# Performance work log

Measured on AMD Instinct MI355X. Metric: run time of the kernel, lower is better.

## Reference

```python
import jax, jax.numpy as jnp
import numpy as np

NEG = -65504.0  # torch.finfo(float16).min
EPS = 1e-6

B, T, D = 2, 1024, 2048
H, HD = 16, 128          # n_head, head_dim
K = 128                  # dynamic_w_hidden_dim
IH = 1                   # dynamic_hidden_dim = H // squeeze_ratio


def _rope(x, freqs_cis):
    # x: [B,T,H,hd]; 'half' mode: first/second half are the rotation pair,
    # output is interleaved (stack(...,-1).flatten(3) in torch).
    half = x.shape[-1] // 2
    a, b = x[..., :half], x[..., half:]
    cos = freqs_cis[None, :, None, :, 0]
    sin = freqs_cis[None, :, None, :, 1]
    out = jnp.stack([a * cos - b * sin, b * cos + a * sin], axis=-1)
    return out.reshape(x.shape)


def _cross_head_proj(inputs, qw1, qw2, kw1, kw2, qdd, kdd):
    # inputs: [B,N,T,S]; qw1/qw2: [B,T,I,N]; kw1/kw2: [B,S,I,N]; qdd: [B,T,N]; kdd: [B,S,N]
    out = inputs
    out = out + jnp.einsum('bnts,btin,btim->bmts', inputs, qw1, qw2)
    out = out + jnp.einsum('bnts,bsin,bsim->bmts', inputs, kw1, kw2)
    out = out + inputs * jnp.swapaxes(qdd, 1, 2)[..., None]   # [B,N,T,1]
    out = out + inputs * jnp.swapaxes(kdd, 1, 2)[:, :, None, :]  # [B,N,1,S]
    return out


def setup_inputs() -> dict:
    key = jax.random.key(0)
    ks = jax.random.split(key, 7)
    x = jax.random.normal(ks[0], (B, T, D), jnp.float32)
    mask = jnp.tril(jnp.ones((1, 1, T, T), bool))  # causal
    # rotary tables: [T, hd/2, 2] (cos, sin)
    inv = 1.0 / (10000.0 ** (jnp.arange(0, HD, 2, dtype=jnp.float32) / HD))
    ang = jnp.arange(T, dtype=jnp.float32)[:, None] * inv[None, :]
    freqs_cis = jnp.stack([jnp.cos(ang), jnp.sin(ang)], axis=-1)
    s = 0.02
    wqkv = jax.random.normal(ks[1], (D, 3 * H * HD), jnp.float32) * s
    wo = jax.random.normal(ks[2], (H * HD, D), jnp.float32) * s
    dw1 = jax.random.normal(ks[3], (D, 4, K), jnp.float32) * s
    qkw = jax.random.normal(ks[4], (4, K, 2 * IH, H), jnp.float32) * s
    dd_w = jax.random.normal(ks[5], (D, 4 * H), jnp.float32) * s
    return {"x": x, "mask": mask, "freqs_cis": freqs_cis, "wqkv": wqkv,
            "wo": wo, "dw1": dw1, "qkw": qkw, "dd_w": dd_w}


def reference(x, mask, freqs_cis, wqkv, wo, dw1, qkw, dd_w):
    b, t, d = x.shape
    qkv = x @ wqkv
    q, k, v = jnp.split(qkv, [H * HD, 2 * H * HD], axis=-1)
    q = q.reshape(b, t, H, HD)
    k = k.reshape(b, t, H, HD)
    v = v.reshape(b, t, H, HD)
    q = _rope(q, freqs_cis)
    k = _rope(k, freqs_cis)
    q = jnp.swapaxes(q, 1, 2) * (HD ** -0.5)  # [B,H,T,hd]
    k = jnp.swapaxes(k, 1, 2)
    v = jnp.swapaxes(v, 1, 2)

    # ---- DynamicWeightProjection (G=1, squeezed) ----
    dw_hidden = jax.nn.gelu(jnp.einsum('btd,dck->btck', x, dw1), approximate=False)
    w = jnp.einsum('btck,ckim->btcim', dw_hidden, qkw)  # [B,T,4,2*IH,H]
    w1, w2 = w[..., :IH, :], w[..., IH:, :]
    w1 = w1 * jax.lax.rsqrt(jnp.mean(w1 * w1, axis=-1, keepdims=True) + EPS)
    pre_qw1, pre_kw1, post_qw1, post_kw1 = [w1[:, :, i] for i in range(4)]
    pre_qw2, pre_kw2, post_qw2, post_kw2 = [w2[:, :, i] for i in range(4)]
    dd = jnp.tanh(x @ dd_w).reshape(b, t, 4, H)
    pre_qdd, pre_kdd, post_qdd, post_kdd = [dd[:, :, i] for i in range(4)]

    # ---- attention with cross-head mixing ----
    logits = jnp.einsum('bhtd,bhsd->bhts', q, k)
    logits = _cross_head_proj(logits, pre_qw1, pre_qw2, pre_kw1, pre_kw2, pre_qdd, pre_kdd)
    logits = jnp.where(mask, logits, NEG)
    probs = jax.nn.softmax(logits, axis=-1)
    probs = _cross_head_proj(probs, post_qw1, post_qw2, post_kw1, post_kw2, post_qdd, post_kdd)
    o = jnp.einsum('bhts,bhsd->bhtd', probs, v)
    o = jnp.swapaxes(o, 1, 2).reshape(b, t, H * HD)
    return o @ wo
```

## Files before the change

kernel.cpp:

```cpp
#include <hip/hip_runtime.h>


typedef unsigned short u16;
typedef unsigned int u32;
typedef __attribute__((ext_vector_type(8))) short s16x8;
typedef __attribute__((ext_vector_type(4))) float f32x4;
typedef __attribute__((ext_vector_type(2))) float f32x2;
typedef __attribute__((ext_vector_type(2))) u16 u16x2;
typedef __attribute__((ext_vector_type(8))) u16 u16x8;

#define DEV __device__ __forceinline__

DEV float bf2f(u16 u) { union { u32 u; float f; } a; a.u = ((u32)u) << 16; return a.f; }
DEV u16 f2bf(float f) {
  union { float f; u32 u; } a; a.f = f;
  u32 r = a.u + 0x7fffu + ((a.u >> 16) & 1u);
  return (u16)(r >> 16);
}

DEV void gload16(const void* g, void* l) {
  __builtin_amdgcn_global_load_lds((__attribute__((address_space(1))) void*)g,
                                   (__attribute__((address_space(3))) void*)l,
                                   16, 0, 0);
}

template <int OUTBF>
__global__ __launch_bounds__(1024, 1) void gemm256(
    const u16* __restrict__ A, const u16* __restrict__ B, void* __restrict__ Cp,
    int K, int lda, int ldb, int ldc)
{
  __shared__ u16 sA[2][256 * 64];
  __shared__ u16 sB[2][256 * 64];
  const int tid = threadIdx.x, ln = tid & 63;
  const int wid = tid >> 6, wm = wid >> 2, wn = wid & 3;

  const int nx = gridDim.x;
  const int fid = blockIdx.y * nx + blockIdx.x;
  const int cpx = (nx * gridDim.y) >> 3;
  const int nid = (fid & 7) * cpx + (fid >> 3);
  const int bx = nid % nx, by = nid / nx;

  const u16* Ab = A + (size_t)(by * 256) * lda;
  const u16* Bb = B + (size_t)(bx * 256) * ldb;

  f32x4 acc[4][4];
#pragma unroll
  for (int m = 0; m < 4; ++m)
#pragma unroll
    for (int n = 0; n < 4; ++n) {
      f32x4 zz = {0.f, 0.f, 0.f, 0.f};
      acc[m][n] = zz;
    }

  int srow[2], scol[2], soff[2];
#pragma unroll
  for (int i = 0; i < 2; ++i) {
    int o = i * 16384 + tid * 16;
    soff[i] = o;
    int r = o >> 7;
    srow[i] = r;
    scol[i] = ((o & 127) ^ ((r & 7) << 4)) >> 1;
  }

#define STAGE_A(ba, k0)                                                   \
  {                                                                       \
    _Pragma("unroll")                                                     \
    for (int i_ = 0; i_ < 2; ++i_)                                        \
      gload16(Ab + (size_t)srow[i_] * lda + (k0) + scol[i_],              \
              (char*)(ba) + soff[i_]);                                    \
  }
#define STAGE_B(bb, k0)                                                   \
  {                                                                       \
    _Pragma("unroll")                                                     \
    for (int i_ = 0; i_ < 2; ++i_)                                        \
      gload16(Bb + (size_t)srow[i_] * ldb + (k0) + scol[i_],              \
              (char*)(bb) + soff[i_]);                                    \
  }

  const int arow = wm * 64 + (ln & 15);
  const int brow = wn * 64 + (ln & 15);
  const int kb = (ln >> 4) * 16;
  const int frswz = (ln & 7) << 4;
  const int NT = K >> 6;

  STAGE_A(sA[0], 0); STAGE_B(sB[0], 0);
  STAGE_A(sA[1], 64); STAGE_B(sB[1], 64);

  for (int t = 0; t < NT; ++t) {
    const int c = t & 1;
    asm volatile("s_waitcnt vmcnt(4)" ::: "memory");
    __builtin_amdgcn_s_barrier();
    const char* pa = (const char*)sA[c];
    const char* pb = (const char*)sB[c];
    s16x8 bfr[4][2];
#pragma unroll
    for (int n = 0; n < 4; ++n)
#pragma unroll
      for (int kk = 0; kk < 2; ++kk)
        bfr[n][kk] = *(const s16x8*)(pb + (size_t)(brow + n * 16) * 128 + ((kk * 64 + kb) ^ frswz));
#pragma unroll
    for (int ph = 0; ph < 4; ++ph) {
      s16x8 afr[2];
#pragma unroll
      for (int kk = 0; kk < 2; ++kk)
        afr[kk] = *(const s16x8*)(pa + (size_t)(arow + ph * 16) * 128 + ((kk * 64 + kb) ^ frswz));
      __builtin_amdgcn_s_setprio(1);
#pragma unroll
      for (int n = 0; n < 4; ++n)
#pragma unroll
        for (int kk = 0; kk < 2; ++kk)
          acc[ph][n] = __builtin_amdgcn_mfma_f32_16x16x32_bf16(
              afr[kk], bfr[n][kk], acc[ph][n], 0, 0, 0);
      __builtin_amdgcn_s_setprio(0);
    }
    __builtin_amdgcn_s_barrier();
    if (t + 2 < NT) { STAGE_A(sA[c], (t + 2) * 64); STAGE_B(sB[c], (t + 2) * 64); }
  }
#undef STAGE_A
#undef STAGE_B

  const int r0 = by * 256 + wm * 64 + ((ln >> 4) << 2);
  const int c0 = bx * 256 + wn * 64 + (ln & 15);
#pragma unroll
  for (int m = 0; m < 4; ++m)
#pragma unroll
    for (int n = 0; n < 4; ++n)
#pragma unroll
      for (int j = 0; j < 4; ++j) {
        int row = r0 + m * 16 + j, col = c0 + n * 16;
        if (OUTBF)
          ((u16*)Cp)[(size_t)row * ldc + col] = f2bf(acc[m][n][j]);
        else
          ((float*)Cp)[(size_t)row * ldc + col] = acc[m][n][j];
      }
}

template <int OUTBF>
__global__ __launch_bounds__(256) void gemm_bt(
    const u16* __restrict__ A, const u16* __restrict__ B, void* __restrict__ Cp,
    int K, int lda, int ldb, int ldc,
    long sAb, long sBb, long sCb1, long sCb2, int CZ2, int cmode, int swz)
{
  int bx = blockIdx.x, by = blockIdx.y;
  if (swz) {
    int nx = gridDim.x;
    int fid = by * nx + bx;
    int cpx = (nx * gridDim.y) >> 3;
    int nid = (fid & 7) * cpx + (fid >> 3);
    bx = nid % nx; by = nid / nx;
  }
  if (cmode == 1 && bx > by) return;
  __shared__ u16 sA[128 * 64];
  __shared__ u16 sB[128 * 64];
  const int tid = threadIdx.x, wv = tid >> 6, ln = tid & 63;
  const int z = blockIdx.z;
  const u16* Ab = A + (size_t)z * sAb + (size_t)(by * 128) * lda;
  const u16* Bb = B + (size_t)z * sBb + (size_t)(bx * 128) * ldb;
  const int wr = (wv >> 1) * 64, wc = (wv & 1) * 64;
  const int Keff = (cmode == 2) ? min(K, (by + 1) * 128) : K;

  f32x4 acc[4][4];
#pragma unroll
  for (int m = 0; m < 4; ++m)
#pragma unroll
    for (int n = 0; n < 4; ++n) {
      f32x4 zz = {0.f, 0.f, 0.f, 0.f};
      acc[m][n] = zz;
    }

  int o_[4], r_[4], cb_[4];
#pragma unroll
  for (int i = 0; i < 4; ++i) {
    int o = (wv * 4 + i) * 1024 + ln * 16;
    o_[i] = o;
    int r = o >> 7;
    r_[i] = r;
    cb_[i] = (o & 127) ^ ((r & 7) << 4);
  }
  const int frswz = (ln & 7) << 4;
  const int fkcol = (ln >> 4) << 4;

  for (int k0 = 0; k0 < Keff; k0 += 64) {
    __syncthreads();
#pragma unroll
    for (int i = 0; i < 4; ++i)
      gload16(Ab + (size_t)r_[i] * lda + (k0 + (cb_[i] >> 1)), (char*)sA + o_[i]);
#pragma unroll
    for (int i = 0; i < 4; ++i)
      gload16(Bb + (size_t)r_[i] * ldb + (k0 + (cb_[i] >> 1)), (char*)sB + o_[i]);
    __syncthreads();

#pragma unroll
    for (int ks = 0; ks < 2; ++ks) {
      s16x8 av[4], bv[4];
#pragma unroll
      for (int m = 0; m < 4; ++m) {
        int row = wr + m * 16 + (ln & 15);
        int addr = row * 128 + ((ks * 64 + fkcol) ^ frswz);
        av[m] = *(const s16x8*)((const char*)sA + addr);
      }
#pragma unroll
      for (int n = 0; n < 4; ++n) {
        int row = wc + n * 16 + (ln & 15);
        int addr = row * 128 + ((ks * 64 + fkcol) ^ frswz);
        bv[n] = *(const s16x8*)((const char*)sB + addr);
      }
#pragma unroll
      for (int m = 0; m < 4; ++m)
#pragma unroll
        for (int n = 0; n < 4; ++n)
          acc[m][n] = __builtin_amdgcn_mfma_f32_16x16x32_bf16(av[m], bv[n], acc[m][n], 0, 0, 0);
    }
  }

  const size_t cbase = (size_t)(z / CZ2) * sCb1 + (size_t)(z % CZ2) * sCb2;
  const int r0 = by * 128 + wr + ((ln >> 4) << 2);
  const int c0 = bx * 128 + wc + (ln & 15);
#pragma unroll
  for (int m = 0; m < 4; ++m)
#pragma unroll
    for (int n = 0; n < 4; ++n)
#pragma unroll
      for (int j = 0; j < 4; ++j) {
        int row = r0 + m * 16 + j, col = c0 + n * 16;
        if (OUTBF)
          ((u16*)Cp)[cbase + (size_t)row * ldc + col] = f2bf(acc[m][n][j]);
        else
          ((float*)Cp)[cbase + (size_t)row * ldc + col] = acc[m][n][j];
      }
}

template <int INBF>
__global__ __launch_bounds__(256) void transpose_to_bf16(
    const void* __restrict__ srcv, u16* __restrict__ dst,
    int R, int C, int Cpad, int srcLd, long sSrc1, long sSrc2, int Z2, long sDst)
{
  __shared__ float tile[32][33];
  const int z = blockIdx.z, z1 = z / Z2, z2 = z % Z2;
  const size_t sbase = (size_t)z1 * sSrc1 + (size_t)z2 * sSrc2;
  u16* d = dst + (size_t)z * sDst;
  const int c0 = blockIdx.x * 32, r0 = blockIdx.y * 32;
  const int tx = threadIdx.x, ty = threadIdx.y;
#pragma unroll
  for (int i = 0; i < 4; ++i) {
    int r = r0 + ty + i * 8, c = c0 + tx;
    float v = 0.f;
    if (c < C && r < R) {
      if (INBF) v = bf2f(((const u16*)srcv)[sbase + (size_t)r * srcLd + c]);
      else      v = ((const float*)srcv)[sbase + (size_t)r * srcLd + c];
    }
    tile[ty + i * 8][tx] = v;
  }
  __syncthreads();
#pragma unroll
  for (int i = 0; i < 4; ++i) {
    int dr = c0 + ty + i * 8, dc = r0 + tx;
    if (dr < Cpad && dc < R) d[(size_t)dr * R + dc] = f2bf(tile[tx][ty + i * 8]);
  }
}

__global__ void cvt_f32_bf16_k(const float* __restrict__ src, u16* __restrict__ dst, int n4) {
  int i = blockIdx.x * 256 + threadIdx.x;
  if (i >= n4) return;
  const float4 v = ((const float4*)src)[i];
  u16* o = dst + (size_t)i * 4;
  o[0] = f2bf(v.x); o[1] = f2bf(v.y); o[2] = f2bf(v.z); o[3] = f2bf(v.w);
}

__global__ __launch_bounds__(256) void rope_k(
    const u16* __restrict__ qkvm, const float* __restrict__ fc,
    u16* __restrict__ qb, u16* __restrict__ kb)
{
  const int bt = blockIdx.x, b = bt >> 10, t = bt & 1023;
  const u16* row = qkvm + (size_t)bt * 6912;
  const float SC = 0.08838834764831845f;
#pragma unroll
  for (int it = 0; it < 4; ++it) {
    int idx = threadIdx.x + it * 256;
    int h = idx >> 6, j = idx & 63;
    float c = fc[(t * 64 + j) * 2], sn = fc[(t * 64 + j) * 2 + 1];
    float qa = bf2f(row[h * 128 + j]), qbv = bf2f(row[h * 128 + 64 + j]);
    float ka = bf2f(row[2048 + h * 128 + j]), kbv = bf2f(row[2048 + h * 128 + 64 + j]);
    size_t o = ((size_t)(b * 16 + h) * 1024 + t) * 128 + 2 * j;
    qb[o]     = f2bf((qa * c - qbv * sn) * SC);
    qb[o + 1] = f2bf((qbv * c + qa * sn) * SC);
    kb[o]     = f2bf(ka * c - kbv * sn);
    kb[o + 1] = f2bf(kbv * c + ka * sn);
  }
}

__global__ __launch_bounds__(64) void gelu_bf16_k(u16* __restrict__ qm) {
  int bt = blockIdx.x, tid = threadIdx.x;
  u16* p = qm + (size_t)bt * 6912 + 6144 + tid * 8;
  u16x8 v = *(u16x8*)p;
#pragma unroll
  for (int i = 0; i < 8; ++i) {
    float f = bf2f(v[i]);
    f = 0.5f * f * (1.f + erff(f * 0.70710678118654752f));
    v[i] = f2bf(f);
  }
  *(u16x8*)p = v;
}

__global__ __launch_bounds__(64) void wproj_k(
    const u16* __restrict__ qkvm, const float* __restrict__ qkw,
    float* __restrict__ w1a, float* __restrict__ w2a, float* __restrict__ kpT)
{
  const int bt = blockIdx.x, ln = threadIdx.x;
  const int c = ln >> 4, m = ln & 15;
  const int b = bt >> 10, t = bt & 1023;
  const u16* hp = qkvm + (size_t)bt * 6912 + 6144 + c * 128;
  const float* Wp = qkw + (size_t)c * 4096 + m;
  float w1 = 0.f, w2 = 0.f;
  for (int k = 0; k < 128; ++k) {
    float hv = bf2f(hp[k]);
    w1 += hv * Wp[k * 32];
    w2 += hv * Wp[k * 32 + 16];
  }
  float ss = w1 * w1;
  ss += __shfl_xor(ss, 1); ss += __shfl_xor(ss, 2);
  ss += __shfl_xor(ss, 4); ss += __shfl_xor(ss, 8);
  float nrm = rsqrtf(ss * (1.f / 16.f) + 1e-6f);
  float w1n = w1 * nrm;
  size_t o = (size_t)bt * 64 + c * 16 + m;
  w1a[o] = w1n;
  w2a[o] = w2;
  size_t kb = (size_t)b * 98304 + (size_t)m * 1024 + t;
  if (c == 1) { kpT[kb] = w1n; kpT[kb + 16384] = w2; }
  if (c == 3) { kpT[kb + 49152] = w1n; kpT[kb + 65536] = w2; }
}

__global__ __launch_bounds__(64) void dd_k(const u16* __restrict__ qkvm,
                                           float* __restrict__ dda, float* __restrict__ kpT) {
  int bt = blockIdx.x, ln = threadIdx.x;
  int c = ln >> 4, m = ln & 15;
  int b = bt >> 10, t = bt & 1023;
  float v = tanhf(bf2f(qkvm[(size_t)bt * 6912 + 6656 + ln]));
  dda[(size_t)bt * 64 + ln] = v;
  size_t kb = (size_t)b * 98304 + (size_t)m * 1024 + t;
  if (c == 1) kpT[kb + 32768] = v;
  if (c == 3) kpT[kb + 81920] = v;
}

__global__ __launch_bounds__(512, 4) void proj_softmax_k(
    const u16* __restrict__ L, u16* __restrict__ P,
    const float* __restrict__ w1a, const float* __restrict__ w2a,
    const float* __restrict__ dda, const float* __restrict__ kparT)
{
  const int t = blockIdx.x, b = blockIdx.y;
  const int tid = threadIdx.x, wv = tid >> 6, ln = tid & 63;
  const int s0 = tid * 2;
  const bool live = (s0 <= t);
  const int sKeff = (t & ~127) + 128;

  __shared__ float tbuf[8][64][17];
  __shared__ float qpar[6][16];
  __shared__ float red2[16][8];
  __shared__ float rzf[16];
  if (tid < 96) {
    int a = tid >> 4, hh = tid & 15;
    const float* sp = (a == 0 || a == 3) ? w1a : ((a == 1 || a == 4) ? w2a : dda);
    int cc = (a < 3) ? 0 : 2;
    qpar[a][hh] = sp[(size_t)(b * 1024 + t) * 64 + cc * 16 + hh];
  }
  __syncthreads();

  const float* kp = kparT + (size_t)b * 98304 + s0;
  float v[16][2];
  const size_t lbase = ((size_t)(b * 16) * 1024 + t) * 1024 + s0;

  if (live) {
#pragma unroll
    for (int h = 0; h < 16; ++h) {
      u16x2 d = *(const u16x2*)(L + lbase + (size_t)h * 1048576);
      v[h][0] = bf2f(d[0]); v[h][1] = bf2f(d[1]);
    }
    float dq0 = 0.f, dq1 = 0.f, dk0 = 0.f, dk1 = 0.f;
#pragma unroll
    for (int h = 0; h < 16; ++h) {
      f32x2 k1 = *(const f32x2*)(kp + h * 1024);
      dq0 += v[h][0] * qpar[0][h]; dq1 += v[h][1] * qpar[0][h];
      dk0 += v[h][0] * k1[0];      dk1 += v[h][1] * k1[1];
    }
    const bool ok1 = (s0 + 1 <= t);
#pragma unroll
    for (int h = 0; h < 16; ++h) {
      f32x2 k2 = *(const f32x2*)(kp + 16384 + h * 1024);
      f32x2 kd = *(const f32x2*)(kp + 32768 + h * 1024);
      float a0 = v[h][0] * (1.f + qpar[2][h] + kd[0]) + qpar[1][h] * dq0 + k2[0] * dk0;
      float a1 = v[h][1] * (1.f + qpar[2][h] + kd[1]) + qpar[1][h] * dq1 + k2[1] * dk1;
      v[h][0] = __expf(a0);
      v[h][1] = ok1 ? __expf(a1) : 0.f;
    }
  }

  {
    float* tb = &tbuf[wv][ln][0];
#pragma unroll
    for (int h = 0; h < 16; ++h)
      tb[h] = live ? (v[h][0] + v[h][1]) : 0.f;
    int hh = ln & 15, q = ln >> 4;
    float sum = 0.f;
#pragma unroll
    for (int k = 0; k < 16; ++k) sum += tbuf[wv][q * 16 + k][hh];
    sum += __shfl_xor(sum, 16);
    sum += __shfl_xor(sum, 32);
    if (ln < 16) red2[ln][wv] = sum;
  }
  __syncthreads();
  if (tid < 16)
    rzf[tid] = 1.f / (((red2[tid][0] + red2[tid][1]) + (red2[tid][2] + red2[tid][3])) +
                      ((red2[tid][4] + red2[tid][5]) + (red2[tid][6] + red2[tid][7])));
  __syncthreads();

  if (s0 >= sKeff) return;

  const size_t pbase = ((size_t)(b * 16) * 1024 + t) * 1024 + s0;
  if (live) {
    float pdq0 = 0.f, pdq1 = 0.f, pdk0 = 0.f, pdk1 = 0.f;
#pragma unroll
    for (int h = 0; h < 16; ++h) {
      float rz = rzf[h];
      f32x2 k1 = *(const f32x2*)(kp + 49152 + h * 1024);
      float p0 = v[h][0] * rz, p1 = v[h][1] * rz;
      v[h][0] = p0; v[h][1] = p1;
      pdq0 += p0 * qpar[3][h]; pdq1 += p1 * qpar[3][h];
      pdk0 += p0 * k1[0];      pdk1 += p1 * k1[1];
    }
#pragma unroll
    for (int h = 0; h < 16; ++h) {
      f32x2 k2 = *(const f32x2*)(kp + 65536 + h * 1024);
      f32x2 kd = *(const f32x2*)(kp + 81920 + h * 1024);
      u16x2 pk;
      pk[0] = f2bf(v[h][0] * (1.f + qpar[5][h] + kd[0]) + qpar[4][h] * pdq0 + k2[0] * pdk0);
      pk[1] = f2bf(v[h][1] * (1.f + qpar[5][h] + kd[1]) + qpar[4][h] * pdq1 + k2[1] * pdk1);
      *(u16x2*)(P + pbase + (size_t)h * 1048576) = pk;
    }
  } else {
    u16x2 z2 = {0, 0};
#pragma unroll
    for (int h = 0; h < 16; ++h)
      *(u16x2*)(P + pbase + (size_t)h * 1048576) = z2;
  }
}

extern "C" void kernel_launch(void* const* d_in, const int* in_sizes, int n_in,
                              void* d_out, int out_size, void* d_ws, size_t ws_size,
                              hipStream_t stream)
{
  (void)in_sizes; (void)n_in; (void)out_size; (void)ws_size;
  const float* x    = (const float*)d_in[0];
  const float* fc   = (const float*)d_in[2];
  const float* wqkv = (const float*)d_in[3];
  const float* wo   = (const float*)d_in[4];
  const float* dw1  = (const float*)d_in[5];
  const float* qkw  = (const float*)d_in[6];
  const float* ddw  = (const float*)d_in[7];
  float* out = (float*)d_out;
  char* w = (char*)d_ws;

  u16*   woT   = (u16*)(w + 0);
  u16*   qb    = (u16*)(w + 8388608);
  u16*   kb    = (u16*)(w + 16777216);
  u16*   vT    = (u16*)(w + 25165824);
  u16*   obf   = (u16*)(w + 33554432);
  float* w1a   = (float*)(w + 41943040);
  float* w2a   = (float*)(w + 42467328);
  float* dda   = (float*)(w + 42991616);
  const size_t TB = 43515904;
  u16*   xb    = (u16*)(w + TB);
  u16*   wallT = (u16*)(w + TB + 8388608);
  u16*   qkvm  = (u16*)(w + TB + 36700160);
  u16*   L     = (u16*)(w + TB);
  u16*   P     = (u16*)(w + TB + 67108864);
  float* kparT = (float*)(w + 244842496);

  cvt_f32_bf16_k<<<4096, 256, 0, stream>>>(x, xb, 1048576);
  transpose_to_bf16<0><<<dim3(192, 64, 1), dim3(32, 8), 0, stream>>>(wqkv, wallT, 2048, 6144, 6144, 6144, 0, 0, 1, 0);
  transpose_to_bf16<0><<<dim3(16, 64, 1),  dim3(32, 8), 0, stream>>>(dw1,  wallT + (size_t)6144 * 2048, 2048, 512, 512, 512, 0, 0, 1, 0);
  transpose_to_bf16<0><<<dim3(8, 64, 1),   dim3(32, 8), 0, stream>>>(ddw,  wallT + (size_t)6656 * 2048, 2048, 64, 256, 64, 0, 0, 1, 0);
  transpose_to_bf16<0><<<dim3(64, 64, 1),  dim3(32, 8), 0, stream>>>(wo,   woT, 2048, 2048, 2048, 2048, 0, 0, 1, 0);

  gemm256<1><<<dim3(27, 8, 1), 1024, 0, stream>>>(xb, wallT, qkvm, 2048, 2048, 2048, 6912);
  rope_k<<<2048, 256, 0, stream>>>(qkvm, fc, qb, kb);
  transpose_to_bf16<1><<<dim3(4, 32, 32), dim3(32, 8), 0, stream>>>(qkvm + 4096, vT, 1024, 128, 128, 6912, 7077888, 128, 16, 131072);

  gelu_bf16_k<<<2048, 64, 0, stream>>>(qkvm);
  wproj_k<<<2048, 64, 0, stream>>>(qkvm, qkw, w1a, w2a, kparT);
  dd_k<<<2048, 64, 0, stream>>>(qkvm, dda, kparT);

  gemm_bt<1><<<dim3(8, 8, 32), 256, 0, stream>>>(qb, kb, L, 128, 128, 128, 1024, 131072, 131072, 1048576, 0, 1, 1, 0);
  proj_softmax_k<<<dim3(1024, 2, 1), 512, 0, stream>>>(L, P, w1a, w2a, dda, kparT);
  gemm_bt<1><<<dim3(1, 8, 32), 256, 0, stream>>>(P, vT, obf, 1024, 1024, 1024, 2048, 1048576, 131072, 2097152, 128, 16, 2, 0);

  gemm_bt<0><<<dim3(16, 16, 1), 256, 0, stream>>>(obf, woT, out, 2048, 2048, 2048, 2048, 0, 0, 0, 0, 1, 0, 1);
}
```

Measured before the change: 271.4 us.

## Shrink QKV GEMM tile to 128x256 with K=32 steps and 2 blocks/CU

The large fused QKV/dw/dd projection GEMM moves from a 256x256 tile with 1024 threads and K-step 64 to a 128x256 tile with 512 threads and K-step 32. The shared-memory staging layout is repacked so that two 32-wide K rows share one swizzled 128-byte line. The smaller LDS footprint and launch bounds of (512, 2) let two blocks share a CU, and the grid doubles from 216 to 432 blocks to fill more CUs. In exchange, each tile reuses fewer A rows, issues more barriers per unit of K, and has a shallower prefetch per stage.

```diff
diff --git a/kernel.cpp b/kernel.cpp
--- a/kernel.cpp
+++ b/kernel.cpp
@@ -25,12 +25,12 @@
 }
 
 template <int OUTBF>
-__global__ __launch_bounds__(1024, 1) void gemm256(
+__global__ __launch_bounds__(512, 2) void gemm256(
     const u16* __restrict__ A, const u16* __restrict__ B, void* __restrict__ Cp,
     int K, int lda, int ldb, int ldc)
 {
-  __shared__ u16 sA[2][256 * 64];
-  __shared__ u16 sB[2][256 * 64];
+  __shared__ u16 sA[2][128 * 32];
+  __shared__ u16 sB[2][256 * 32];
   const int tid = threadIdx.x, ln = tid & 63;
   const int wid = tid >> 6, wm = wid >> 2, wn = wid & 3;
 
@@ -40,7 +40,7 @@
   const int nid = (fid & 7) * cpx + (fid >> 3);
   const int bx = nid % nx, by = nid / nx;
 
-  const u16* Ab = A + (size_t)(by * 256) * lda;
+  const u16* Ab = A + (size_t)(by * 128) * lda;
   const u16* Bb = B + (size_t)(bx * 256) * ldb;
 
   f32x4 acc[4][4];
@@ -52,74 +52,75 @@
       acc[m][n] = zz;
     }
 
-  int srow[2], scol[2], soff[2];
+  int saro, sarow, sacol;
+  {
+    int o = tid * 16;
+    saro = o;
+    int r = o >> 7;
+    int swz = (o & 127) ^ ((r & 7) << 4);
+    sarow = 2 * r + (swz >> 6);
+    sacol = (swz & 63) >> 1;
+  }
+  int sbro[2], sbrow[2], sbcol[2];
 #pragma unroll
   for (int i = 0; i < 2; ++i) {
-    int o = i * 16384 + tid * 16;
-    soff[i] = o;
+    int o = i * 8192 + tid * 16;
+    sbro[i] = o;
     int r = o >> 7;
-    srow[i] = r;
-    scol[i] = ((o & 127) ^ ((r & 7) << 4)) >> 1;
+    int swz = (o & 127) ^ ((r & 7) << 4);
+    sbrow[i] = 2 * r + (swz >> 6);
+    sbcol[i] = (swz & 63) >> 1;
   }
 
 #define STAGE_A(ba, k0)                                                   \
-  {                                                                       \
-    _Pragma("unroll")                                                     \
-    for (int i_ = 0; i_ < 2; ++i_)                                        \
-      gload16(Ab + (size_t)srow[i_] * lda + (k0) + scol[i_],              \
-              (char*)(ba) + soff[i_]);                                    \
-  }
+  gload16(Ab + (size_t)sarow * lda + (k0) + sacol, (char*)(ba) + saro);
 #define STAGE_B(bb, k0)                                                   \
   {                                                                       \
     _Pragma("unroll")                                                     \
     for (int i_ = 0; i_ < 2; ++i_)                                        \
-      gload16(Bb + (size_t)srow[i_] * ldb + (k0) + scol[i_],              \
-              (char*)(bb) + soff[i_]);                                    \
-  }
-
-  const int arow = wm * 64 + (ln & 15);
-  const int brow = wn * 64 + (ln & 15);
-  const int kb = (ln >> 4) * 16;
-  const int frswz = (ln & 7) << 4;
-  const int NT = K >> 6;
+      gload16(Bb + (size_t)sbrow[i_] * ldb + (k0) + sbcol[i_],            \
+              (char*)(bb) + sbro[i_]);                                    \
+  }
+
+  const int kbyte = (ln >> 4) * 16;
+  const int arw = wm * 64 + (ln & 15);
+  const int brw = wn * 64 + (ln & 15);
+  const int NT = K >> 5;
+
+#define RD(p, R)                                                          \
+  (*(const s16x8*)((const char*)(p) + (size_t)((R) >> 1) * 128 +          \
+                   ((((R) & 1) * 64 + kbyte) ^ ((((R) >> 1) & 7) << 4))))
 
   STAGE_A(sA[0], 0); STAGE_B(sB[0], 0);
-  STAGE_A(sA[1], 64); STAGE_B(sB[1], 64);
+  STAGE_A(sA[1], 32); STAGE_B(sB[1], 32);
 
   for (int t = 0; t < NT; ++t) {
     const int c = t & 1;
-    asm volatile("s_waitcnt vmcnt(4)" ::: "memory");
+    asm volatile("s_waitcnt vmcnt(3)" ::: "memory");
     __builtin_amdgcn_s_barrier();
-    const char* pa = (const char*)sA[c];
-    const char* pb = (const char*)sB[c];
-    s16x8 bfr[4][2];
+    const u16* pa = sA[c];
+    const u16* pb = sB[c];
+    s16x8 bfr[4];
 #pragma unroll
     for (int n = 0; n < 4; ++n)
-#pragma unroll
-      for (int kk = 0; kk < 2; ++kk)
-        bfr[n][kk] = *(const s16x8*)(pb + (size_t)(brow + n * 16) * 128 + ((kk * 64 + kb) ^ frswz));
-#pragma unroll
-    for (int ph = 0; ph < 4; ++ph) {
-      s16x8 afr[2];
-#pragma unroll
-      for (int kk = 0; kk < 2; ++kk)
-        afr[kk] = *(const s16x8*)(pa + (size_t)(arow + ph * 16) * 128 + ((kk * 64 + kb) ^ frswz));
+      bfr[n] = RD(pb, brw + n * 16);
+#pragma unroll
+    for (int m = 0; m < 4; ++m) {
+      s16x8 afr = RD(pa, arw + m * 16);
       __builtin_amdgcn_s_setprio(1);
 #pragma unroll
       for (int n = 0; n < 4; ++n)
-#pragma unroll
-        for (int kk = 0; kk < 2; ++kk)
-          acc[ph][n] = __builtin_amdgcn_mfma_f32_16x16x32_bf16(
-              afr[kk], bfr[n][kk], acc[ph][n], 0, 0, 0);
+        acc[m][n] = __builtin_amdgcn_mfma_f32_16x16x32_bf16(afr, bfr[n], acc[m][n], 0, 0, 0);
       __builtin_amdgcn_s_setprio(0);
     }
     __builtin_amdgcn_s_barrier();
-    if (t + 2 < NT) { STAGE_A(sA[c], (t + 2) * 64); STAGE_B(sB[c], (t + 2) * 64); }
+    if (t + 2 < NT) { STAGE_A(sA[c], (t + 2) * 32); STAGE_B(sB[c], (t + 2) * 32); }
   }
 #undef STAGE_A
 #undef STAGE_B
-
-  const int r0 = by * 256 + wm * 64 + ((ln >> 4) << 2);
+#undef RD
+
+  const int r0 = by * 128 + wm * 64 + ((ln >> 4) << 2);
   const int c0 = bx * 256 + wn * 64 + (ln & 15);
 #pragma unroll
   for (int m = 0; m < 4; ++m)
@@ -481,7 +482,7 @@
   transpose_to_bf16<0><<<dim3(8, 64, 1),   dim3(32, 8), 0, stream>>>(ddw,  wallT + (size_t)6656 * 2048, 2048, 64, 256, 64, 0, 0, 1, 0);
   transpose_to_bf16<0><<<dim3(64, 64, 1),  dim3(32, 8), 0, stream>>>(wo,   woT, 2048, 2048, 2048, 2048, 0, 0, 1, 0);
 
-  gemm256<1><<<dim3(27, 8, 1), 1024, 0, stream>>>(xb, wallT, qkvm, 2048, 2048, 2048, 6912);
+  gemm256<1><<<dim3(27, 16, 1), 512, 0, stream>>>(xb, wallT, qkvm, 2048, 2048, 2048, 6912);
   rope_k<<<2048, 256, 0, stream>>>(qkvm, fc, qb, kb);
   transpose_to_bf16<1><<<dim3(4, 32, 32), dim3(32, 8), 0, stream>>>(qkvm + 4096, vT, 1024, 128, 128, 6912, 7077888, 128, 16, 131072);
 
```

Measured after the change: 279.4 us. 2.9% more time.
